# Kernel tuning notes

Measured on AMD Instinct MI355X. Metric: run time of the kernel, lower is better.

The kernel has to match this reference:

```python
import jax, jax.numpy as jnp
import numpy as np

EMBED = 256
HEADS = 8
HD = EMBED // HEADS
LEVELS = 4
POINTS = 4
FFN_H = 1024
BS = 8
LQ = 900
SHAPES = [(100, 100), (50, 50), (25, 25), (13, 13)]


def setup_inputs() -> dict:
    key = jax.random.key(0)
    ks = jax.random.split(key, 20)
    nv = sum(h * w for h, w in SHAPES)
    starts = np.cumsum([0] + [h * w for h, w in SHAPES])[:-1]
    inp = {
        "queries": jax.random.normal(ks[0], (BS, LQ, EMBED), jnp.float32),
        "memory": jax.random.normal(ks[1], (BS, nv, EMBED), jnp.float32),
        "query_pos": jax.random.normal(ks[2], (BS, LQ, EMBED), jnp.float32),
        "reference_points": jax.random.uniform(ks[3], (BS, LQ, LEVELS, 4), jnp.float32) * 0.9 + 0.05,
        "spatial_shapes": jnp.asarray(SHAPES, jnp.int32),
        "level_start_index": jnp.asarray(starts, jnp.int32),
    }
    def lin(k, din, dout):
        k1, k2 = jax.random.split(k)
        w = jax.random.normal(k1, (din, dout), jnp.float32) * 0.02
        b = jax.random.normal(k2, (dout,), jnp.float32) * 0.01
        return w, b
    specs = [("Wq", "bq", EMBED, EMBED), ("Wk", "bk", EMBED, EMBED), ("Wv", "bv", EMBED, EMBED),
             ("Wo", "bo", EMBED, EMBED), ("Wvd", "bvd", EMBED, EMBED),
             ("Woff", "boff", EMBED, HEADS * LEVELS * POINTS * 2),
             ("Watt", "batt", EMBED, HEADS * LEVELS * POINTS),
             ("Wop", "bop", EMBED, EMBED), ("Wg", "bg", 2 * EMBED, 2 * EMBED),
             ("W1", "b1", EMBED, FFN_H), ("W2", "b2", FFN_H, EMBED)]
    for i, (wn, bn, di, do) in enumerate(specs):
        w, b = lin(ks[4 + i], di, do)
        inp[wn] = w
        inp[bn] = b
    for n in ["ln1", "ln2", "ln3"]:
        inp[n + "_s"] = jnp.ones((EMBED,), jnp.float32)
        inp[n + "_b"] = jnp.zeros((EMBED,), jnp.float32)
    return inp


def _ln(x, s, b):
    m = jnp.mean(x, -1, keepdims=True)
    v = jnp.mean(jnp.square(x - m), -1, keepdims=True)
    return (x - m) * jax.lax.rsqrt(v + 1e-5) * s + b


def _bilinear(v_l, lx, ly, H, W):
    # v_l: [bs,h,H*W,hd]; lx,ly: [bs,h,lq,p] normalized in [0,1]
    # grid_sample(align_corners=False, padding=zeros) semantics
    px = lx * W - 0.5
    py = ly * H - 0.5
    x0 = jnp.floor(px)
    y0 = jnp.floor(py)
    wx = px - x0
    wy = py - y0
    x0i = x0.astype(jnp.int32)
    y0i = y0.astype(jnp.int32)
    bs, h, lq, p = lx.shape
    out = jnp.zeros((bs, h, lq, p, HD), v_l.dtype)
    for dy in (0, 1):
        for dx in (0, 1):
            xi = x0i + dx
            yi = y0i + dy
            w = (wx if dx else 1.0 - wx) * (wy if dy else 1.0 - wy)
            valid = (xi >= 0) & (xi < W) & (yi >= 0) & (yi < H)
            idx = jnp.clip(yi, 0, H - 1) * W + jnp.clip(xi, 0, W - 1)
            g = jnp.take_along_axis(v_l, idx.reshape(bs, h, lq * p)[..., None], axis=2)
            g = g.reshape(bs, h, lq, p, HD)
            out = out + w[..., None] * jnp.where(valid[..., None], g, 0.0)
    return out


def reference(queries, memory, query_pos, reference_points, spatial_shapes, level_start_index,
              Wq, bq, Wk, bk, Wv, bv, Wo, bo, Wvd, bvd, Woff, boff, Watt, batt, Wop, bop,
              Wg, bg, W1, b1, W2, b2, ln1_s, ln1_b, ln2_s, ln2_b, ln3_s, ln3_b):
    bs, lq, _ = queries.shape
    shp = np.asarray(spatial_shapes)
    st = np.asarray(level_start_index)

    # ---- self attention (pre-norm, q=k=x+pos, v=x) ----
    x = _ln(queries, ln1_s, ln1_b)
    qk = x + query_pos
    Q = (qk @ Wq + bq).reshape(bs, lq, HEADS, HD)
    K = (qk @ Wk + bk).reshape(bs, lq, HEADS, HD)
    V = (x @ Wv + bv).reshape(bs, lq, HEADS, HD)
    scores = jnp.einsum('bqhd,bkhd->bhqk', Q, K) * (1.0 / np.sqrt(HD))
    attn = jax.nn.softmax(scores, axis=-1)
    sa = jnp.einsum('bhqk,bkhd->bqhd', attn, V).reshape(bs, lq, EMBED) @ Wo + bo
    x1 = queries + sa  # dropout is identity in eval

    # ---- MS-deformable cross attention ----
    y = _ln(x1, ln2_s, ln2_b)
    qc = y + query_pos
    val = (memory @ Wvd + bvd).reshape(bs, -1, HEADS, HD).transpose(0, 2, 1, 3)  # [bs,h,Nv,hd]
    off = (qc @ Woff + boff).reshape(bs, lq, HEADS, LEVELS, POINTS, 2)
    aw = jax.nn.softmax((qc @ Watt + batt).reshape(bs, lq, HEADS, LEVELS * POINTS), axis=-1)
    aw = aw.reshape(bs, lq, HEADS, LEVELS, POINTS)
    rp = reference_points[:, :, None, :, None, :]  # [bs,lq,1,L,1,4]
    loc = rp[..., :2] + off / POINTS * rp[..., 2:] * 0.5  # [bs,lq,h,L,p,2]

    out = jnp.zeros((bs, HEADS, lq, HD), queries.dtype)
    for l in range(LEVELS):
        H, W = int(shp[l, 0]), int(shp[l, 1])
        s0 = int(st[l])
        v_l = val[:, :, s0:s0 + H * W]
        lx = jnp.transpose(loc[:, :, :, l, :, 0], (0, 2, 1, 3))  # [bs,h,lq,p]
        ly = jnp.transpose(loc[:, :, :, l, :, 1], (0, 2, 1, 3))
        samp = _bilinear(v_l, lx, ly, H, W)  # [bs,h,lq,p,hd]
        w = jnp.transpose(aw[:, :, :, l], (0, 2, 1, 3))  # [bs,h,lq,p]
        out = out + jnp.sum(w[..., None] * samp, axis=3)
    cross = out.transpose(0, 2, 1, 3).reshape(bs, lq, EMBED) @ Wop + bop

    # ---- gated fusion ----
    gi = jnp.concatenate([x1, cross], axis=-1)
    g = jax.nn.sigmoid(gi @ Wg + bg)
    x2 = g[..., :EMBED] * x1 + g[..., EMBED:] * cross

    # ---- FFN ----
    z = _ln(x2, ln3_s, ln3_b)
    ffn = jax.nn.relu(z @ W1 + b1) @ W2 + b2
    return (x2 + ffn, aw, loc)
```

## Files before the change

### kernel.cpp

```cpp
#include <hip/hip_runtime.h>
#include <hip/hip_bf16.h>
#include <math.h>

#define BB 8
#define LQ 900
#define EE 256
#define NH 8
#define HD 32
#define NL 4
#define NP 4
#define FFN_H 1024

typedef __bf16 bf16x8 __attribute__((ext_vector_type(8)));
typedef float f32x4 __attribute__((ext_vector_type(4)));
typedef unsigned short u16x8 __attribute__((ext_vector_type(8)));

__device__ __forceinline__ unsigned short f2b(float f) {
    union { float f; unsigned int u; } v; v.f = f;
    unsigned int u = v.u;
    unsigned int r = (u + 0x7fffu + ((u >> 16) & 1u)) >> 16;
    return (unsigned short)r;
}
__device__ __forceinline__ float b2f(unsigned short h) {
    union { unsigned int u; float f; } v; v.u = ((unsigned int)h) << 16; return v.f;
}

typedef __attribute__((address_space(3))) unsigned int* lds_ptr_t;
typedef const __attribute__((address_space(1))) unsigned int* gbl_ptr_t;
#define GLOAD16(g, l) __builtin_amdgcn_global_load_lds((gbl_ptr_t)(g), (lds_ptr_t)(l), 16, 0, 0)
#define VMCNT(n) asm volatile("s_waitcnt vmcnt(" #n ")" ::: "memory")
#define LGKM0()  asm volatile("s_waitcnt lgkmcnt(0)" ::: "memory")

struct TDesc { const float* src; unsigned short* dst; int K, N, tile0; };
struct TPack {
    TDesc d[12];
    const float *bq, *bk, *boff, *batt;
    float *bqk, *boa;
    const float *Wop_src, *Wg_src, *bop_src, *bg_src;
    unsigned short* WopRow;
    float* bgg;
};

__global__ __launch_bounds__(256) void prep_kernel(
    TPack p,
    const float* __restrict__ queries, const float* __restrict__ qpos,
    const float* __restrict__ ln1_s, const float* __restrict__ ln1_b,
    unsigned short* __restrict__ x_b, unsigned short* __restrict__ qk_b,
    const float* __restrict__ mem, unsigned short* __restrict__ mem_b, long memN)
{
    const int bi = blockIdx.x;
    const int t = threadIdx.x;

    if (bi < 1248) {
        int di = 0;
#pragma unroll
        for (int i = 1; i < 12; ++i) if (bi >= p.d[i].tile0) di = i;
        TDesc d = p.d[di];
        int tt = bi - d.tile0;
        int tn = (d.N + 31) >> 5;
        int tk = tt / tn, tc = tt % tn;
        __shared__ float tile[32][33];
        int tx = t & 31, ty = t >> 5;
#pragma unroll
        for (int i = 0; i < 4; ++i) {
            int kk = tk * 32 + ty + i * 8, nn = tc * 32 + tx;
            tile[ty + i * 8][tx] = d.src[(size_t)kk * d.N + nn];
        }
        __syncthreads();
#pragma unroll
        for (int i = 0; i < 4; ++i) {
            int nn = tc * 32 + ty + i * 8, kk = tk * 32 + tx;
            d.dst[(size_t)nn * d.K + kk] = f2b(tile[tx][ty + i * 8]);
        }
        return;
    }
    if (bi < 1252) {
        int which = bi - 1248;
        if (which == 0)      p.bqk[t] = p.bq[t];
        else if (which == 1) p.bqk[256 + t] = p.bk[t];
        else if (which == 2) p.boa[t] = p.boff[t];
        else if (t < 128)    p.boa[256 + t] = p.batt[t];
        return;
    }
    if (bi < 1284) {
        long i = ((long)(bi - 1252) * 256 + t) * 8;
        float4 a = *(const float4*)(p.Wop_src + i);
        float4 b = *(const float4*)(p.Wop_src + i + 4);
        u16x8 o;
        o[0] = f2b(a.x); o[1] = f2b(a.y); o[2] = f2b(a.z); o[3] = f2b(a.w);
        o[4] = f2b(b.x); o[5] = f2b(b.y); o[6] = f2b(b.z); o[7] = f2b(b.w);
        *(u16x8*)(p.WopRow + i) = o;
        return;
    }
    if (bi < 1286) {
        int n = (bi - 1284) * 256 + t;
        float bb = p.bg_src[n];
        for (int j = 0; j < 256; ++j)
            bb += p.bop_src[j] * p.Wg_src[(size_t)(256 + j) * 512 + n];
        p.bgg[n] = bb;
        return;
    }
    if (bi < 8486) {
        const int row = bi - 1286;
        const int w = t >> 6, lane = t & 63;
        __shared__ float red[4];
        float v = queries[(size_t)row * EE + t];
        float sum = v;
#pragma unroll
        for (int o = 32; o; o >>= 1) sum += __shfl_xor(sum, o, 64);
        if (lane == 0) red[w] = sum;
        __syncthreads();
        float mean = (red[0] + red[1] + red[2] + red[3]) * (1.0f / 256.0f);
        __syncthreads();
        float dd = v - mean;
        float sq = dd * dd;
#pragma unroll
        for (int o = 32; o; o >>= 1) sq += __shfl_xor(sq, o, 64);
        if (lane == 0) red[w] = sq;
        __syncthreads();
        float var = (red[0] + red[1] + red[2] + red[3]) * (1.0f / 256.0f);
        float y = dd * rsqrtf(var + 1e-5f) * ln1_s[t] + ln1_b[t];
        x_b[(size_t)row * EE + t]  = f2b(y);
        qk_b[(size_t)row * EE + t] = f2b(y + qpos[(size_t)row * EE + t]);
        return;
    }
    {
        long i = ((long)(bi - 8486) * 256 + t) * 8;
        long stride = (long)2048 * 256 * 8;
        for (; i < memN; i += stride) {
            float4 a = *(const float4*)(mem + i);
            float4 b = *(const float4*)(mem + i + 4);
            u16x8 o;
            o[0] = f2b(a.x); o[1] = f2b(a.y); o[2] = f2b(a.z); o[3] = f2b(a.w);
            o[4] = f2b(b.x); o[5] = f2b(b.y); o[6] = f2b(b.z); o[7] = f2b(b.w);
            *(u16x8*)(mem_b + i) = o;
        }
    }
}

struct GD {
    const unsigned short* A;
    const float* Af;
    const unsigned short* Bt;
    const float* bias;
    const float* resid;
    float* outF;
    unsigned short* outB;
    const float* lnS; const float* lnB; const float* lnAdd;
    unsigned short* lnOut;
    int M, K, N, ntN, tile0, ldOutB, outBoff, act, aF32, ldA;
};
struct GB { GD d[4]; int nd, tot; };

template<int BN>
__global__ __launch_bounds__(256, (BN == 128) ? 4 : 2) void gemm_pipe(GB g) {
    __shared__ __align__(16) unsigned short ldsb[2][(64 + BN) * 32];
    __shared__ float lnred[2][64][2];
    const int tid = threadIdx.x;
    const int l = tid & 63, w = tid >> 6;
    const int wr = w >> 1, wc = w & 1;
    constexpr int NJ = BN / 32;

    int t = blockIdx.x;
    if (t >= g.tot) return;
    int d = 0;
    while (d + 1 < g.nd && t >= g.d[d + 1].tile0) ++d;

    const int sc = tid & 3;
    float4 fA[2];

    auto stage = [&](int dd, int tt, int ks, int pp) {
        const GD& D = g.d[dd];
        const int lda = D.ldA ? D.ldA : D.K;
        int local = tt - D.tile0;
        int m0 = (local / D.ntN) * 64;
        int n0 = (local % D.ntN) * BN;
        unsigned short* base = &ldsb[pp][0];
        if (D.aF32) {
            int row = tid >> 2;
            int rg = m0 + row; int mm = D.M - 1; rg = rg < mm ? rg : mm;
            int ck = (sc ^ ((row >> 1) & 3)) * 8;
            const float* src = D.Af + (size_t)rg * lda + (ks << 5) + ck;
            fA[0] = *(const float4*)src;
            fA[1] = *(const float4*)(src + 4);
        } else {
            int row = w * 16 + (l >> 2);
            int rg = m0 + row; int mm = D.M - 1; rg = rg < mm ? rg : mm;
            int schunk = ((l & 3) ^ ((row >> 1) & 3)) << 4;
            GLOAD16((const char*)(D.A + (size_t)rg * lda + (ks << 5)) + schunk,
                    base + (w * 16) * 32);
        }
#pragma unroll
        for (int ib = 0; ib < BN / 64; ++ib) {
            int row = ib * 64 + w * 16 + (l >> 2);
            int rg = n0 + row; int nn = D.N - 1; rg = rg < nn ? rg : nn;
            int schunk = ((l & 3) ^ ((row >> 1) & 3)) << 4;
            GLOAD16((const char*)(D.Bt + (size_t)rg * D.K + (ks << 5)) + schunk,
                    base + 2048 + (ib * 64 + w * 16) * 32);
        }
    };
    auto commitA = [&](int pp) {
        int row = tid >> 2;
        u16x8 o;
        o[0] = f2b(fA[0].x); o[1] = f2b(fA[0].y); o[2] = f2b(fA[0].z); o[3] = f2b(fA[0].w);
        o[4] = f2b(fA[1].x); o[5] = f2b(fA[1].y); o[6] = f2b(fA[1].z); o[7] = f2b(fA[1].w);
        *(u16x8*)((char*)&ldsb[pp][0] + row * 64 + sc * 16) = o;
    };

    stage(d, t, 0, 0);
    if (g.d[d].aF32) { commitA(0); LGKM0(); }
    int p = 0;

    while (true) {
        const GD D = g.d[d];
        int local = t - D.tile0;
        const int m0 = (local / D.ntN) * 64;
        const int n0 = (local % D.ntN) * BN;
        const int nk = D.K >> 5;

        f32x4 acc[2][NJ];
#pragma unroll
        for (int i = 0; i < 2; ++i)
#pragma unroll
            for (int j = 0; j < NJ; ++j) acc[i][j] = (f32x4){0.f, 0.f, 0.f, 0.f};

        for (int ks = 0; ks < nk; ++ks) {
            int nt = t, nks = ks + 1, ndd = d;
            bool have = true;
            if (nks == nk) {
                nt = t + gridDim.x; nks = 0;
                if (nt >= g.tot) have = false;
                else { while (ndd + 1 < g.nd && nt >= g.d[ndd + 1].tile0) ++ndd; }
            }
            bool stagedAF = have && g.d[ndd].aF32;
            if (have) {
                stage(ndd, nt, nks, p ^ 1);
                if (stagedAF) {
                    if constexpr (BN == 128) { VMCNT(4); } else { VMCNT(6); }
                } else {
                    if constexpr (BN == 128) { VMCNT(3); } else { VMCNT(5); }
                }
            } else {
                VMCNT(0);
            }
            __builtin_amdgcn_sched_barrier(0);
            __builtin_amdgcn_s_barrier();
            __builtin_amdgcn_sched_barrier(0);
            {
                const char* base = (const char*)&ldsb[p][0];
                const int rch = ((l >> 4) ^ ((l >> 1) & 3)) << 4;
                bf16x8 af[2];
#pragma unroll
                for (int i = 0; i < 2; ++i) {
                    int row = wr * 32 + i * 16 + (l & 15);
                    af[i] = *(const bf16x8*)(base + row * 64 + rch);
                }
#pragma unroll
                for (int j = 0; j < NJ; ++j) {
                    int row = wc * (BN / 2) + j * 16 + (l & 15);
                    bf16x8 bfr = *(const bf16x8*)(base + 4096 + row * 64 + rch);
#pragma unroll
                    for (int i = 0; i < 2; ++i)
                        acc[i][j] = __builtin_amdgcn_mfma_f32_16x16x32_bf16(af[i], bfr, acc[i][j], 0, 0, 0);
                }
            }
            if (stagedAF) { commitA(p ^ 1); LGKM0(); }
            __builtin_amdgcn_sched_barrier(0);
            __builtin_amdgcn_s_barrier();
            __builtin_amdgcn_sched_barrier(0);
            p ^= 1;
        }

#pragma unroll
        for (int i = 0; i < 2; ++i) {
#pragma unroll
            for (int r = 0; r < 4; ++r) {
                int gm = m0 + wr * 32 + i * 16 + ((l >> 4) << 2) + r;
                if (gm >= D.M) continue;
#pragma unroll
                for (int j = 0; j < NJ; ++j) {
                    int gn = n0 + wc * (BN / 2) + j * 16 + (l & 15);
                    if (gn >= D.N) continue;
                    float v = acc[i][j][r];
                    if (D.bias)  v += D.bias[gn];
                    if (D.resid) v += D.resid[(size_t)gm * D.N + gn];
                    if (D.act == 1)      v = fmaxf(v, 0.f);
                    else if (D.act == 2) v = 1.0f / (1.0f + __expf(-v));
                    acc[i][j][r] = v;
                    if (D.outF) D.outF[(size_t)gm * D.N + gn] = v;
                    if (D.outB) D.outB[(size_t)gm * D.ldOutB + D.outBoff + gn] = f2b(v);
                }
            }
        }

        if constexpr (BN == 256) {
            if (D.lnOut) {
#pragma unroll
                for (int i = 0; i < 2; ++i) {
#pragma unroll
                    for (int r = 0; r < 4; ++r) {
                        float s1 = 0.f, s2 = 0.f;
#pragma unroll
                        for (int j = 0; j < NJ; ++j) {
                            float v = acc[i][j][r];
                            s1 += v; s2 += v * v;
                        }
#pragma unroll
                        for (int o = 1; o <= 8; o <<= 1) {
                            s1 += __shfl_xor(s1, o, 64);
                            s2 += __shfl_xor(s2, o, 64);
                        }
                        if ((l & 15) == 0) {
                            int row = wr * 32 + i * 16 + ((l >> 4) << 2) + r;
                            lnred[wc][row][0] = s1;
                            lnred[wc][row][1] = s2;
                        }
                    }
                }
                __syncthreads();
#pragma unroll
                for (int i = 0; i < 2; ++i) {
#pragma unroll
                    for (int r = 0; r < 4; ++r) {
                        int row = wr * 32 + i * 16 + ((l >> 4) << 2) + r;
                        int gm = m0 + row;
                        if (gm >= D.M) continue;
                        float mean = (lnred[0][row][0] + lnred[1][row][0]) * (1.0f / 256.0f);
                        float msq  = (lnred[0][row][1] + lnred[1][row][1]) * (1.0f / 256.0f);
                        float rs = rsqrtf(msq - mean * mean + 1e-5f);
#pragma unroll
                        for (int j = 0; j < NJ; ++j) {
                            int gn = wc * (BN / 2) + j * 16 + (l & 15);
                            float y = (acc[i][j][r] - mean) * rs * D.lnS[gn] + D.lnB[gn]
                                      + D.lnAdd[(size_t)gm * 256 + gn];
                            D.lnOut[(size_t)gm * 256 + gn] = f2b(y);
                        }
                    }
                }
            }
        }

        t += gridDim.x;
        if (t >= g.tot) break;
        while (d + 1 < g.nd && t >= g.d[d + 1].tile0) ++d;
    }
}

__global__ __launch_bounds__(256) void attn_mfma(
    const unsigned short* __restrict__ QK, const unsigned short* __restrict__ Vb,
    unsigned short* __restrict__ outB)
{
    const int qt = blockIdx.x;
    const int bh = blockIdx.y;
    const int b = bh >> 3, h = bh & 7;
    const int tid = threadIdx.x;
    const int w = tid >> 6, l = tid & 63;

    __shared__ __align__(16) unsigned short Ks[64 * 32];
    __shared__ __align__(16) unsigned short VT[32 * 64];
    __shared__ __align__(16) unsigned short Ps[4][64 * 20];

    const int qrow_w = qt * 64 + w * 16;
    int qr = qrow_w + (l & 15); qr = qr < LQ ? qr : LQ - 1;
    bf16x8 qf = *(const bf16x8*)(QK + ((size_t)(b * LQ + qr)) * 512 + h * 32 + (l >> 4) * 8);

    f32x4 acc0 = {0.f, 0.f, 0.f, 0.f}, acc1 = {0.f, 0.f, 0.f, 0.f};
    float m_run = -1e30f, l_run = 0.f;
    const float scale = 0.17677669529663689f;
    const f32x4 z4 = {0.f, 0.f, 0.f, 0.f};

    const int key = tid >> 2;
    const int dg = (tid & 3) * 8;
    u16x8 kvc, vvc, kvn, vvn;
    {
        int krow = key; krow = krow < LQ ? krow : LQ - 1;
        size_t base = (size_t)(b * LQ + krow);
        kvc = *(const u16x8*)(QK + base * 512 + 256 + h * 32 + dg);
        vvc = *(const u16x8*)(Vb + base * 256 + h * 32 + dg);
    }

    for (int kt = 0; kt < 15; ++kt) {
        __syncthreads();
        *(u16x8*)((char*)Ks + key * 64 + ((dg * 2) ^ ((key & 3) << 4))) = kvc;
#pragma unroll
        for (int e = 0; e < 8; ++e) {
            int dd = dg + e;
            *(unsigned short*)((char*)VT + dd * 128 + ((key * 2) ^ ((dd & 7) << 4))) = vvc[e];
        }
        if (kt < 14) {
            int krow = (kt + 1) * 64 + key; krow = krow < LQ ? krow : LQ - 1;
            size_t base = (size_t)(b * LQ + krow);
            kvn = *(const u16x8*)(QK + base * 512 + 256 + h * 32 + dg);
            vvn = *(const u16x8*)(Vb + base * 256 + h * 32 + dg);
        }
        __syncthreads();

        float p[4][4];
        float tmax = -1e30f;
#pragma unroll
        for (int m = 0; m < 4; ++m) {
            int kr = m * 16 + (l & 15);
            bf16x8 kf = *(const bf16x8*)((const char*)Ks + kr * 64 +
                        (((l >> 4) * 16) ^ ((kr & 3) << 4)));
            f32x4 sf = __builtin_amdgcn_mfma_f32_16x16x32_bf16(kf, qf, z4, 0, 0, 0);
#pragma unroll
            for (int r = 0; r < 4; ++r) {
                int kk = kt * 64 + m * 16 + (l >> 4) * 4 + r;
                float sv = (kk < LQ) ? sf[r] * scale : -1e30f;
                p[m][r] = sv;
                tmax = fmaxf(tmax, sv);
            }
        }
        tmax = fmaxf(tmax, __shfl_xor(tmax, 16, 64));
        tmax = fmaxf(tmax, __shfl_xor(tmax, 32, 64));
        float newm = fmaxf(m_run, tmax);
        float corr = __expf(m_run - newm);
        m_run = newm;
        float tsum = 0.f;
#pragma unroll
        for (int m = 0; m < 4; ++m)
#pragma unroll
            for (int r = 0; r < 4; ++r) {
                float e = __expf(p[m][r] - newm);
                p[m][r] = e;
                tsum += e;
            }
        tsum += __shfl_xor(tsum, 16, 64);
        tsum += __shfl_xor(tsum, 32, 64);
        l_run = l_run * corr + tsum;
        acc0 *= corr;
        acc1 *= corr;

        unsigned short* pw = &Ps[w][0];
#pragma unroll
        for (int m = 0; m < 4; ++m)
#pragma unroll
            for (int r = 0; r < 4; ++r) {
                int kk = m * 16 + (l >> 4) * 4 + r;
                pw[kk * 20 + (l & 15)] = f2b(p[m][r]);
            }

#pragma unroll
        for (int s = 0; s < 2; ++s) {
            union { unsigned short u[8]; bf16x8 v; } pb;
#pragma unroll
            for (int j = 0; j < 8; ++j)
                pb.u[j] = pw[(s * 32 + (l >> 4) * 8 + j) * 20 + (l & 15)];
#pragma unroll
            for (int m2 = 0; m2 < 2; ++m2) {
                int dd = m2 * 16 + (l & 15);
                bf16x8 vf = *(const bf16x8*)((const char*)VT + dd * 128 +
                            ((s * 64 + (l >> 4) * 16) ^ ((dd & 7) << 4)));
                if (m2 == 0) acc0 = __builtin_amdgcn_mfma_f32_16x16x32_bf16(vf, pb.v, acc0, 0, 0, 0);
                else         acc1 = __builtin_amdgcn_mfma_f32_16x16x32_bf16(vf, pb.v, acc1, 0, 0, 0);
            }
        }
        if (kt < 14) { kvc = kvn; vvc = vvn; }
    }

    float inv = 1.0f / l_run;
    int q = qrow_w + (l & 15);
    if (q < LQ) {
        size_t obase = ((size_t)(b * LQ + q)) * 256 + h * 32;
#pragma unroll
        for (int r = 0; r < 4; ++r) {
            int d0 = (l >> 4) * 4 + r;
            outB[obase + d0]      = f2b(acc0[r] * inv);
            outB[obase + 16 + d0] = f2b(acc1[r] * inv);
        }
    }
}

__global__ __launch_bounds__(256) void sample_fused(
    const float* __restrict__ off_att, const float* __restrict__ refp,
    const unsigned short* __restrict__ val,
    const int* __restrict__ shapes, const int* __restrict__ starts,
    float* __restrict__ aw_out, float* __restrict__ loc_out,
    unsigned short* __restrict__ xs, int NV)
{
    const int row = blockIdx.x;
    const int b = row / LQ;
    const int t = threadIdx.x;
    const int h = t >> 5, d = t & 31;

    __shared__ float l_logit[128];
    __shared__ float l_aw[128];
    __shared__ float l_loc[256];
    __shared__ int l_sh[NL * 2];
    __shared__ int l_st[NL];

    if (t < 128) l_logit[t] = off_att[(size_t)row * 384 + 256 + t];
    {
        float o = off_att[(size_t)row * 384 + t];
        int c = t & 1;
        int lv = (t >> 3) & 3;
        float rc = refp[((size_t)row * 4 + lv) * 4 + c];
        float rs = refp[((size_t)row * 4 + lv) * 4 + 2 + c];
        float loc = rc + o * 0.125f * rs;
        l_loc[t] = loc;
        loc_out[(size_t)row * 256 + t] = loc;
    }
    if (t < NL * 2) l_sh[t] = shapes[t];
    if (t < NL) l_st[t] = starts[t];
    __syncthreads();
    if (t < 128) {
        int hh = t >> 4;
        float mx = -1e30f;
#pragma unroll
        for (int i = 0; i < 16; ++i) mx = fmaxf(mx, l_logit[hh * 16 + i]);
        float sum = 0.f;
#pragma unroll
        for (int i = 0; i < 16; ++i) sum += __expf(l_logit[hh * 16 + i] - mx);
        float aw = __expf(l_logit[t] - mx) / sum;
        l_aw[t] = aw;
        aw_out[(size_t)row * 128 + t] = aw;
    }
    __syncthreads();

    float acc = 0.f;
    const unsigned short* vb = val + (size_t)b * NV * EE + h * HD + d;

#pragma unroll
    for (int lv = 0; lv < NL; ++lv) {
        const int Hh = l_sh[lv * 2], Ww = l_sh[lv * 2 + 1];
        const int s0 = l_st[lv];
#pragma unroll
        for (int p = 0; p < NP; ++p) {
            const int base = ((h * NL + lv) * NP + p) * 2;
            float lx = l_loc[base], ly = l_loc[base + 1];
            float wgt0 = l_aw[h * 16 + lv * NP + p];
            float px = lx * (float)Ww - 0.5f;
            float py = ly * (float)Hh - 0.5f;
            float x0f = floorf(px), y0f = floorf(py);
            float wx = px - x0f, wy = py - y0f;
            int x0 = (int)x0f, y0 = (int)y0f;
#pragma unroll
            for (int dy = 0; dy < 2; ++dy) {
                int yi = y0 + dy;
                bool vy = (yi >= 0) && (yi < Hh);
                int yc = min(max(yi, 0), Hh - 1);
                float wyv = dy ? wy : 1.f - wy;
#pragma unroll
                for (int dx = 0; dx < 2; ++dx) {
                    int xi = x0 + dx;
                    bool vv = vy && (xi >= 0) && (xi < Ww);
                    int xc = min(max(xi, 0), Ww - 1);
                    float wgt = wgt0 * wyv * (dx ? wx : 1.f - wx);
                    float gv = b2f(vb[(size_t)(s0 + yc * Ww + xc) * EE]);
                    acc += vv ? wgt * gv : 0.f;
                }
            }
        }
    }
    xs[(size_t)row * 512 + 256 + t] = f2b(acc);
}

__global__ __launch_bounds__(256) void gate_ln3(
    const float* __restrict__ g, const float* __restrict__ x1,
    const float* __restrict__ cross, const float* __restrict__ s,
    const float* __restrict__ bln, float* __restrict__ x2out,
    unsigned short* __restrict__ zb)
{
    const int row = blockIdx.x;
    const int t = threadIdx.x;
    const int w = t >> 6;
    const int lane = t & 63;
    __shared__ float red[4];

    float g1 = g[(size_t)row * 512 + t];
    float g2 = g[(size_t)row * 512 + 256 + t];
    float v = g1 * x1[(size_t)row * EE + t] + g2 * cross[(size_t)row * EE + t];
    x2out[(size_t)row * EE + t] = v;

    float sum = v;
#pragma unroll
    for (int o = 32; o; o >>= 1) sum += __shfl_xor(sum, o, 64);
    if (lane == 0) red[w] = sum;
    __syncthreads();
    float mean = (red[0] + red[1] + red[2] + red[3]) * (1.0f / 256.0f);
    __syncthreads();

    float d = v - mean;
    float sq = d * d;
#pragma unroll
    for (int o = 32; o; o >>= 1) sq += __shfl_xor(sq, o, 64);
    if (lane == 0) red[w] = sq;
    __syncthreads();
    float var = (red[0] + red[1] + red[2] + red[3]) * (1.0f / 256.0f);

    float y = d * rsqrtf(var + 1e-5f) * s[t] + bln[t];
    zb[(size_t)row * EE + t] = f2b(y);
}

extern "C" void kernel_launch(void* const* d_in, const int* in_sizes, int n_in,
                              void* d_out, int out_size, void* d_ws, size_t ws_size,
                              hipStream_t stream)
{
    const float* queries   = (const float*)d_in[0];
    const float* memory    = (const float*)d_in[1];
    const float* query_pos = (const float*)d_in[2];
    const float* refp      = (const float*)d_in[3];
    const int*   shapes    = (const int*)d_in[4];
    const int*   starts    = (const int*)d_in[5];
    const float* Wq  = (const float*)d_in[6],  *bq  = (const float*)d_in[7];
    const float* Wk  = (const float*)d_in[8],  *bk  = (const float*)d_in[9];
    const float* Wv  = (const float*)d_in[10], *bv  = (const float*)d_in[11];
    const float* Wo  = (const float*)d_in[12], *bo  = (const float*)d_in[13];
    const float* Wvd = (const float*)d_in[14], *bvd = (const float*)d_in[15];
    const float* Woff= (const float*)d_in[16], *boff= (const float*)d_in[17];
    const float* Watt= (const float*)d_in[18], *batt= (const float*)d_in[19];
    const float* Wop = (const float*)d_in[20], *bop = (const float*)d_in[21];
    const float* Wg  = (const float*)d_in[22], *bg  = (const float*)d_in[23];
    const float* W1  = (const float*)d_in[24], *b1  = (const float*)d_in[25];
    const float* W2  = (const float*)d_in[26], *b2  = (const float*)d_in[27];
    const float* ln1_s = (const float*)d_in[28], *ln1_b = (const float*)d_in[29];
    const float* ln2_s = (const float*)d_in[30], *ln2_b = (const float*)d_in[31];
    const float* ln3_s = (const float*)d_in[32], *ln3_b = (const float*)d_in[33];

    const int NV = in_sizes[1] / (BB * EE);
    const int Mq = BB * LQ;
    const int Mv = BB * NV;
    const long memN = (long)Mv * EE;

    char* W8 = (char*)d_ws;
    size_t off = 0;
    auto alloc = [&](size_t bytes) { char* p = W8 + off; off += (bytes + 255) & ~(size_t)255; return p; };

    unsigned short* mem_b = (unsigned short*)alloc((size_t)memN * 2);
    unsigned short* val_b = (unsigned short*)alloc((size_t)memN * 2);
    unsigned short* WtQK  = (unsigned short*)alloc(512 * 256 * 2);
    unsigned short* WtV   = (unsigned short*)alloc(256 * 256 * 2);
    unsigned short* WtO   = (unsigned short*)alloc(256 * 256 * 2);
    unsigned short* WtVD  = (unsigned short*)alloc(256 * 256 * 2);
    unsigned short* WtOA  = (unsigned short*)alloc(384 * 256 * 2);
    unsigned short* WtOP  = (unsigned short*)alloc(256 * 256 * 2);
    unsigned short* WtGF  = (unsigned short*)alloc(512 * 512 * 2);
    unsigned short* Wg2T  = (unsigned short*)alloc(512 * 256 * 2);
    unsigned short* WopRow= (unsigned short*)alloc(256 * 256 * 2);
    unsigned short* Wt1   = (unsigned short*)alloc(1024 * 256 * 2);
    unsigned short* Wt2   = (unsigned short*)alloc(256 * 1024 * 2);
    float*          bqk   = (float*)alloc(512 * 4);
    float*          boa   = (float*)alloc(384 * 4);
    float*          bgg   = (float*)alloc(512 * 4);
    unsigned short* qkb   = (unsigned short*)alloc((size_t)Mq * 512 * 2);
    unsigned short* vb_buf= (unsigned short*)alloc((size_t)Mq * 256 * 2);
    unsigned short* av_buf= (unsigned short*)alloc((size_t)Mq * 256 * 2);
    float*          x1    = (float*)alloc((size_t)Mq * 256 * 4);
    unsigned short* xs_cat= (unsigned short*)alloc((size_t)Mq * 512 * 2);
    unsigned short* qc_b  = (unsigned short*)alloc((size_t)Mq * 256 * 2);
    unsigned short* qk_b  = (unsigned short*)alloc((size_t)Mq * 256 * 2);
    float*          cross = (float*)alloc((size_t)Mq * 256 * 4);

    unsigned short* x_b = (unsigned short*)cross;
    float* off_att = (float*)qkb;
    float* gbuf = (float*)mem_b;
    float* x2   = (float*)((char*)mem_b + (size_t)Mq * 512 * 4);
    unsigned short* z_b = (unsigned short*)((char*)x2 + (size_t)Mq * 256 * 4);
    unsigned short* hidden_b = (unsigned short*)((char*)z_b + (size_t)Mq * 256 * 2);

    float* out0    = (float*)d_out;
    float* aw_out  = out0 + (size_t)Mq * 256;
    float* loc_out = aw_out + (size_t)Mq * 128;

    dim3 blk(256);
    const int tMq = (Mq + 63) / 64;
    const int tv  = (Mv + 63) / 64;

    TPack tp;
    tp.d[0]  = { Wq,             WtQK,             256, 256,    0 };
    tp.d[1]  = { Wk,             WtQK + 256 * 256, 256, 256,   64 };
    tp.d[2]  = { Wv,             WtV,              256, 256,  128 };
    tp.d[3]  = { Wo,             WtO,              256, 256,  192 };
    tp.d[4]  = { Wvd,            WtVD,             256, 256,  256 };
    tp.d[5]  = { Woff,           WtOA,             256, 256,  320 };
    tp.d[6]  = { Watt,           WtOA + 256 * 256, 256, 128,  384 };
    tp.d[7]  = { Wop,            WtOP,             256, 256,  416 };
    tp.d[8]  = { Wg,             WtGF,             512, 512,  480 };
    tp.d[9]  = { Wg + 256 * 512, Wg2T,             256, 512,  608 };
    tp.d[10] = { W1,             Wt1,              256, 1024, 736 };
    tp.d[11] = { W2,             Wt2,             1024, 256,  992 };
    tp.bq = bq; tp.bk = bk; tp.boff = boff; tp.batt = batt;
    tp.bqk = bqk; tp.boa = boa;
    tp.Wop_src = Wop; tp.Wg_src = Wg; tp.bop_src = bop; tp.bg_src = bg;
    tp.WopRow = WopRow; tp.bgg = bgg;
    prep_kernel<<<10534, blk, 0, stream>>>(
        tp, queries, query_pos, ln1_s, ln1_b, x_b, qk_b, memory, mem_b, memN);

    {
        GB g; g.nd = 4;
        g.d[0] = { mem_b, nullptr, WtVD, bvd, nullptr, nullptr, val_b,
                   nullptr, nullptr, nullptr, nullptr,
                   Mv, 256, 256, 2, 0, 256, 0, 0, 0, 0 };
        g.d[1] = { qk_b, nullptr, WtQK, bqk, nullptr, nullptr, qkb,
                   nullptr, nullptr, nullptr, nullptr,
                   Mq, 256, 512, 4, tv * 2, 512, 0, 0, 0, 0 };
        g.d[2] = { x_b, nullptr, WtV, bv, nullptr, nullptr, vb_buf,
                   nullptr, nullptr, nullptr, nullptr,
                   Mq, 256, 256, 2, tv * 2 + tMq * 4, 256, 0, 0, 0, 0 };
        g.d[3] = { Wg2T, nullptr, WopRow, nullptr, nullptr, nullptr, WtGF,
                   nullptr, nullptr, nullptr, nullptr,
                   512, 256, 256, 2, tv * 2 + tMq * 6, 512, 256, 0, 0, 0 };
        g.tot = tv * 2 + tMq * 6 + 16;
        gemm_pipe<128><<<1536, blk, 0, stream>>>(g);
    }

    attn_mfma<<<dim3(15, BB * NH), blk, 0, stream>>>(qkb, vb_buf, av_buf);

    {
        GB g; g.nd = 1;
        g.d[0] = { av_buf, nullptr, WtO, bo, queries, x1, xs_cat,
                   ln2_s, ln2_b, query_pos, qc_b,
                   Mq, 256, 256, 1, 0, 512, 0, 0, 0, 0 };
        g.tot = tMq;
        gemm_pipe<256><<<tMq, blk, 0, stream>>>(g);
    }

    {
        GB g; g.nd = 1;
        g.d[0] = { qc_b, nullptr, WtOA, boa, nullptr, off_att, nullptr,
                   nullptr, nullptr, nullptr, nullptr,
                   Mq, 256, 384, 3, 0, 384, 0, 0, 0, 0 };
        g.tot = tMq * 3;
        gemm_pipe<128><<<g.tot, blk, 0, stream>>>(g);
    }

    sample_fused<<<Mq, blk, 0, stream>>>(off_att, refp, val_b, shapes, starts,
                                         aw_out, loc_out, xs_cat, NV);

    {
        GB g; g.nd = 2;
        g.d[0] = { xs_cat + 256, nullptr, WtOP, bop, nullptr, cross, nullptr,
                   nullptr, nullptr, nullptr, nullptr,
                   Mq, 256, 256, 2, 0, 0, 0, 0, 0, 512 };
        g.d[1] = { xs_cat, nullptr, WtGF, bgg, nullptr, gbuf, nullptr,
                   nullptr, nullptr, nullptr, nullptr,
                   Mq, 512, 512, 4, tMq * 2, 0, 0, 2, 0, 0 };
        g.tot = tMq * 6;
        gemm_pipe<128><<<g.tot, blk, 0, stream>>>(g);
    }

    gate_ln3<<<Mq, blk, 0, stream>>>(gbuf, x1, cross, ln3_s, ln3_b, x2, z_b);

    {
        GB g; g.nd = 1;
        g.d[0] = { z_b, nullptr, Wt1, b1, nullptr, nullptr, hidden_b,
                   nullptr, nullptr, nullptr, nullptr,
                   Mq, 256, 1024, 8, 0, 1024, 0, 1, 0, 0 };
        g.tot = tMq * 8;
        gemm_pipe<128><<<g.tot, blk, 0, stream>>>(g);
    }

    {
        GB g; g.nd = 1;
        g.d[0] = { hidden_b, nullptr, Wt2, b2, x2, out0, nullptr,
                   nullptr, nullptr, nullptr, nullptr,
                   Mq, 1024, 256, 2, 0, 256, 0, 0, 0, 0 };
        g.tot = tMq * 2;
        gemm_pipe<128><<<g.tot, blk, 0, stream>>>(g);
    }
}
```

Before: 339.2 us.

## Deepen GEMM pipeline to three LDS stages and drop unused fp32-A path

Switches the persistent GEMM from double to triple buffering for BN=128 tiles. It tracks a staging cursor that runs ahead of the compute cursor across k-steps and tiles, and it picks the vmcnt wait from the number of stages in flight. It also removes the unused fp32-A conversion path and its struct fields. The aim is to hide more global-load latency, at the cost of 50% more LDS per block, which may lower occupancy against launch_bounds 4. The LN epilogue column index changes to wc*128, which is only correct for the BN=256 case that uses it.

```diff
diff --git a/kernel.cpp b/kernel.cpp
--- a/kernel.cpp
+++ b/kernel.cpp
@@ -29,7 +29,6 @@
 typedef const __attribute__((address_space(1))) unsigned int* gbl_ptr_t;
 #define GLOAD16(g, l) __builtin_amdgcn_global_load_lds((gbl_ptr_t)(g), (lds_ptr_t)(l), 16, 0, 0)
 #define VMCNT(n) asm volatile("s_waitcnt vmcnt(" #n ")" ::: "memory")
-#define LGKM0()  asm volatile("s_waitcnt lgkmcnt(0)" ::: "memory")
 
 struct TDesc { const float* src; unsigned short* dst; int K, N, tile0; };
 struct TPack {
@@ -140,7 +139,6 @@
 
 struct GD {
     const unsigned short* A;
-    const float* Af;
     const unsigned short* Bt;
     const float* bias;
     const float* resid;
@@ -148,13 +146,14 @@
     unsigned short* outB;
     const float* lnS; const float* lnB; const float* lnAdd;
     unsigned short* lnOut;
-    int M, K, N, ntN, tile0, ldOutB, outBoff, act, aF32, ldA;
+    int M, K, N, ntN, tile0, ldOutB, outBoff, act, ldA;
 };
 struct GB { GD d[4]; int nd, tot; };
 
 template<int BN>
 __global__ __launch_bounds__(256, (BN == 128) ? 4 : 2) void gemm_pipe(GB g) {
-    __shared__ __align__(16) unsigned short ldsb[2][(64 + BN) * 32];
+    constexpr int STAGES = (BN == 128) ? 3 : 2;
+    __shared__ __align__(16) unsigned short ldsb[STAGES][(64 + BN) * 32];
     __shared__ float lnred[2][64][2];
     const int tid = threadIdx.x;
     const int l = tid & 63, w = tid >> 6;
@@ -165,9 +164,6 @@
     if (t >= g.tot) return;
     int d = 0;
     while (d + 1 < g.nd && t >= g.d[d + 1].tile0) ++d;
-
-    const int sc = tid & 3;
-    float4 fA[2];
 
     auto stage = [&](int dd, int tt, int ks, int pp) {
         const GD& D = g.d[dd];
@@ -176,14 +172,7 @@
         int m0 = (local / D.ntN) * 64;
         int n0 = (local % D.ntN) * BN;
         unsigned short* base = &ldsb[pp][0];
-        if (D.aF32) {
-            int row = tid >> 2;
-            int rg = m0 + row; int mm = D.M - 1; rg = rg < mm ? rg : mm;
-            int ck = (sc ^ ((row >> 1) & 3)) * 8;
-            const float* src = D.Af + (size_t)rg * lda + (ks << 5) + ck;
-            fA[0] = *(const float4*)src;
-            fA[1] = *(const float4*)(src + 4);
-        } else {
+        {
             int row = w * 16 + (l >> 2);
             int rg = m0 + row; int mm = D.M - 1; rg = rg < mm ? rg : mm;
             int schunk = ((l & 3) ^ ((row >> 1) & 3)) << 4;
@@ -199,17 +188,24 @@
                     base + 2048 + (ib * 64 + w * 16) * 32);
         }
     };
-    auto commitA = [&](int pp) {
-        int row = tid >> 2;
-        u16x8 o;
-        o[0] = f2b(fA[0].x); o[1] = f2b(fA[0].y); o[2] = f2b(fA[0].z); o[3] = f2b(fA[0].w);
-        o[4] = f2b(fA[1].x); o[5] = f2b(fA[1].y); o[6] = f2b(fA[1].z); o[7] = f2b(fA[1].w);
-        *(u16x8*)((char*)&ldsb[pp][0] + row * 64 + sc * 16) = o;
+
+    int st_t = t, st_ks = 0, st_d = d;
+    bool st_valid = true;
+    auto advance = [&]() {
+        ++st_ks;
+        if (st_ks == (g.d[st_d].K >> 5)) {
+            st_ks = 0;
+            st_t += gridDim.x;
+            if (st_t >= g.tot) { st_valid = false; }
+            else { while (st_d + 1 < g.nd && st_t >= g.d[st_d + 1].tile0) ++st_d; }
+        }
     };
 
-    stage(d, t, 0, 0);
-    if (g.d[d].aF32) { commitA(0); LGKM0(); }
-    int p = 0;
+    int sp = 0, cp = 0, nf = 0;
+    stage(st_d, st_t, st_ks, sp); sp = (sp + 1 == STAGES) ? 0 : sp + 1; ++nf; advance();
+    if (STAGES == 3 && st_valid) {
+        stage(st_d, st_t, st_ks, sp); sp = (sp + 1 == STAGES) ? 0 : sp + 1; ++nf; advance();
+    }
 
     while (true) {
         const GD D = g.d[d];
@@ -225,29 +221,19 @@
             for (int j = 0; j < NJ; ++j) acc[i][j] = (f32x4){0.f, 0.f, 0.f, 0.f};
 
         for (int ks = 0; ks < nk; ++ks) {
-            int nt = t, nks = ks + 1, ndd = d;
-            bool have = true;
-            if (nks == nk) {
-                nt = t + gridDim.x; nks = 0;
-                if (nt >= g.tot) have = false;
-                else { while (ndd + 1 < g.nd && nt >= g.d[ndd + 1].tile0) ++ndd; }
-            }
-            bool stagedAF = have && g.d[ndd].aF32;
-            if (have) {
-                stage(ndd, nt, nks, p ^ 1);
-                if (stagedAF) {
-                    if constexpr (BN == 128) { VMCNT(4); } else { VMCNT(6); }
-                } else {
-                    if constexpr (BN == 128) { VMCNT(3); } else { VMCNT(5); }
-                }
-            } else {
-                VMCNT(0);
-            }
+            if (st_valid && nf < STAGES) {
+                stage(st_d, st_t, st_ks, sp);
+                sp = (sp + 1 == STAGES) ? 0 : sp + 1;
+                ++nf; advance();
+            }
+            if (nf == 3)      { VMCNT(6); }
+            else if (nf == 2) { if constexpr (BN == 128) { VMCNT(3); } else { VMCNT(5); } }
+            else              { VMCNT(0); }
             __builtin_amdgcn_sched_barrier(0);
             __builtin_amdgcn_s_barrier();
             __builtin_amdgcn_sched_barrier(0);
             {
-                const char* base = (const char*)&ldsb[p][0];
+                const char* base = (const char*)&ldsb[cp][0];
                 const int rch = ((l >> 4) ^ ((l >> 1) & 3)) << 4;
                 bf16x8 af[2];
 #pragma unroll
@@ -264,11 +250,11 @@
                         acc[i][j] = __builtin_amdgcn_mfma_f32_16x16x32_bf16(af[i], bfr, acc[i][j], 0, 0, 0);
                 }
             }
-            if (stagedAF) { commitA(p ^ 1); LGKM0(); }
             __builtin_amdgcn_sched_barrier(0);
             __builtin_amdgcn_s_barrier();
             __builtin_amdgcn_sched_barrier(0);
-            p ^= 1;
+            cp = (cp + 1 == STAGES) ? 0 : cp + 1;
+            --nf;
         }
 
 #pragma unroll
@@ -330,7 +316,7 @@
                         float rs = rsqrtf(msq - mean * mean + 1e-5f);
 #pragma unroll
                         for (int j = 0; j < NJ; ++j) {
-                            int gn = wc * (BN / 2) + j * 16 + (l & 15);
+                            int gn = wc * 128 + j * 16 + (l & 15);
                             float y = (acc[i][j][r] - mean) * rs * D.lnS[gn] + D.lnB[gn]
                                       + D.lnAdd[(size_t)gm * 256 + gn];
                             D.lnOut[(size_t)gm * 256 + gn] = f2b(y);
@@ -688,18 +674,18 @@
 
     {
         GB g; g.nd = 4;
-        g.d[0] = { mem_b, nullptr, WtVD, bvd, nullptr, nullptr, val_b,
-                   nullptr, nullptr, nullptr, nullptr,
-                   Mv, 256, 256, 2, 0, 256, 0, 0, 0, 0 };
-        g.d[1] = { qk_b, nullptr, WtQK, bqk, nullptr, nullptr, qkb,
-                   nullptr, nullptr, nullptr, nullptr,
-                   Mq, 256, 512, 4, tv * 2, 512, 0, 0, 0, 0 };
-        g.d[2] = { x_b, nullptr, WtV, bv, nullptr, nullptr, vb_buf,
-                   nullptr, nullptr, nullptr, nullptr,
-                   Mq, 256, 256, 2, tv * 2 + tMq * 4, 256, 0, 0, 0, 0 };
-        g.d[3] = { Wg2T, nullptr, WopRow, nullptr, nullptr, nullptr, WtGF,
-                   nullptr, nullptr, nullptr, nullptr,
-                   512, 256, 256, 2, tv * 2 + tMq * 6, 512, 256, 0, 0, 0 };
+        g.d[0] = { mem_b, WtVD, bvd, nullptr, nullptr, val_b,
+                   nullptr, nullptr, nullptr, nullptr,
+                   Mv, 256, 256, 2, 0, 256, 0, 0, 0 };
+        g.d[1] = { qk_b, WtQK, bqk, nullptr, nullptr, qkb,
+                   nullptr, nullptr, nullptr, nullptr,
+                   Mq, 256, 512, 4, tv * 2, 512, 0, 0, 0 };
+        g.d[2] = { x_b, WtV, bv, nullptr, nullptr, vb_buf,
+                   nullptr, nullptr, nullptr, nullptr,
+                   Mq, 256, 256, 2, tv * 2 + tMq * 4, 256, 0, 0, 0 };
+        g.d[3] = { Wg2T, WopRow, nullptr, nullptr, nullptr, WtGF,
+                   nullptr, nullptr, nullptr, nullptr,
+                   512, 256, 256, 2, tv * 2 + tMq * 6, 512, 256, 0, 0 };
         g.tot = tv * 2 + tMq * 6 + 16;
         gemm_pipe<128><<<1536, blk, 0, stream>>>(g);
     }
@@ -708,18 +694,18 @@
 
     {
         GB g; g.nd = 1;
-        g.d[0] = { av_buf, nullptr, WtO, bo, queries, x1, xs_cat,
+        g.d[0] = { av_buf, WtO, bo, queries, x1, xs_cat,
                    ln2_s, ln2_b, query_pos, qc_b,
-                   Mq, 256, 256, 1, 0, 512, 0, 0, 0, 0 };
+                   Mq, 256, 256, 1, 0, 512, 0, 0, 0 };
         g.tot = tMq;
         gemm_pipe<256><<<tMq, blk, 0, stream>>>(g);
     }
 
     {
         GB g; g.nd = 1;
-        g.d[0] = { qc_b, nullptr, WtOA, boa, nullptr, off_att, nullptr,
-                   nullptr, nullptr, nullptr, nullptr,
-                   Mq, 256, 384, 3, 0, 384, 0, 0, 0, 0 };
+        g.d[0] = { qc_b, WtOA, boa, nullptr, off_att, nullptr,
+                   nullptr, nullptr, nullptr, nullptr,
+                   Mq, 256, 384, 3, 0, 384, 0, 0, 0 };
         g.tot = tMq * 3;
         gemm_pipe<128><<<g.tot, blk, 0, stream>>>(g);
     }
@@ -729,12 +715,12 @@
 
     {
         GB g; g.nd = 2;
-        g.d[0] = { xs_cat + 256, nullptr, WtOP, bop, nullptr, cross, nullptr,
-                   nullptr, nullptr, nullptr, nullptr,
-                   Mq, 256, 256, 2, 0, 0, 0, 0, 0, 512 };
-        g.d[1] = { xs_cat, nullptr, WtGF, bgg, nullptr, gbuf, nullptr,
-                   nullptr, nullptr, nullptr, nullptr,
-                   Mq, 512, 512, 4, tMq * 2, 0, 0, 2, 0, 0 };
+        g.d[0] = { xs_cat + 256, WtOP, bop, nullptr, cross, nullptr,
+                   nullptr, nullptr, nullptr, nullptr,
+                   Mq, 256, 256, 2, 0, 0, 0, 0, 512 };
+        g.d[1] = { xs_cat, WtGF, bgg, nullptr, gbuf, nullptr,
+                   nullptr, nullptr, nullptr, nullptr,
+                   Mq, 512, 512, 4, tMq * 2, 0, 0, 2, 0 };
         g.tot = tMq * 6;
         gemm_pipe<128><<<g.tot, blk, 0, stream>>>(g);
     }
@@ -743,18 +729,18 @@
 
     {
         GB g; g.nd = 1;
-        g.d[0] = { z_b, nullptr, Wt1, b1, nullptr, nullptr, hidden_b,
-                   nullptr, nullptr, nullptr, nullptr,
-                   Mq, 256, 1024, 8, 0, 1024, 0, 1, 0, 0 };
+        g.d[0] = { z_b, Wt1, b1, nullptr, nullptr, hidden_b,
+                   nullptr, nullptr, nullptr, nullptr,
+                   Mq, 256, 1024, 8, 0, 1024, 0, 1, 0 };
         g.tot = tMq * 8;
         gemm_pipe<128><<<g.tot, blk, 0, stream>>>(g);
     }
 
     {
         GB g; g.nd = 1;
-        g.d[0] = { hidden_b, nullptr, Wt2, b2, x2, out0, nullptr,
-                   nullptr, nullptr, nullptr, nullptr,
-                   Mq, 1024, 256, 2, 0, 256, 0, 0, 0, 0 };
+        g.d[0] = { hidden_b, Wt2, b2, x2, out0, nullptr,
+                   nullptr, nullptr, nullptr, nullptr,
+                   Mq, 1024, 256, 2, 0, 256, 0, 0, 0 };
         g.tot = tMq * 2;
         gemm_pipe<128><<<g.tot, blk, 0, stream>>>(g);
     }
```

New measurement: 346.4 us. 2.1% more time.
